# Kernel optimization log

Hardware: AMD Instinct MI355X
Metric: run time of the kernel (lower is better)

The kernel has to match this reference:

```python
import jax, jax.numpy as jnp
import numpy as np

D_MODEL = 1024
NHEAD = 16
D_K = D_MODEL // NHEAD


def setup_inputs() -> dict:
    key = jax.random.key(0)
    ks = jax.random.split(key, 10)
    B, S = 2, 2048
    x = jax.random.normal(ks[0], (B, S, D_MODEL), dtype=jnp.float32)
    # sorted 1-D coordinate grid in [0,1], shape [S,1,1] so coords.shape[1]==1
    coords = jnp.sort(jax.random.uniform(ks[1], (S, 1, 1), dtype=jnp.float32), axis=0)
    sc = 1.0 / np.sqrt(D_MODEL)
    Wq = jax.random.normal(ks[2], (D_MODEL, D_MODEL), dtype=jnp.float32) * sc
    bq = jnp.zeros((D_MODEL,), jnp.float32)
    Wk = jax.random.normal(ks[3], (D_MODEL, D_MODEL), dtype=jnp.float32) * sc
    bk = jnp.zeros((D_MODEL,), jnp.float32)
    Wv = jax.random.normal(ks[4], (D_MODEL, D_MODEL), dtype=jnp.float32) * sc
    bv = jnp.zeros((D_MODEL,), jnp.float32)
    Wo = jax.random.normal(ks[5], (D_MODEL, D_MODEL), dtype=jnp.float32) * sc
    bo = jnp.zeros((D_MODEL,), jnp.float32)
    return {"x": x, "coords": coords, "Wq": Wq, "bq": bq, "Wk": Wk, "bk": bk,
            "Wv": Wv, "bv": bv, "Wo": Wo, "bo": bo}


def _split_heads(t):  # [B,S,D] -> [B,H,S,Dk]
    B, S, _ = t.shape
    return t.reshape(B, S, NHEAD, D_K).transpose(0, 2, 1, 3)


def reference(x, coords, Wq, bq, Wk, bk, Wv, bv, Wo, bo):
    B, S, _ = x.shape
    Q = _split_heads(x @ Wq.T + bq)
    K = _split_heads(x @ Wk.T + bk)
    V = _split_heads(x @ Wv.T + bv)

    scale = jnp.sqrt(jnp.float32(D_K))
    scores = jnp.einsum('bhld,bhsd->bhls', Q, K) / scale  # [B,H,S,S]

    # trapezoidal quadrature weights from coord grid: [S-1] -> broadcast shapes
    dc = jnp.abs(coords[1:] - coords[:-1]).reshape(1, 1, 1, S - 1)  # key-axis

    # custom trapezoidal softmax
    e = jnp.exp(scores - jnp.max(scores, axis=-1, keepdims=True))
    denom = jnp.sum(0.5 * dc * (e[..., 1:] + e[..., :-1]), axis=-1, keepdims=True)
    aw = e / denom  # [B,H,S,S]

    dcv = dc.reshape(1, 1, S - 1, 1)  # value-axis weighting
    o1 = jnp.einsum('bhls,bhsd->bhld', aw[..., 1:], dcv * V[:, :, 1:, :])
    o2 = jnp.einsum('bhls,bhsd->bhld', aw[..., :-1], dcv * V[:, :, :-1, :])
    out = 0.5 * (o1 + o2)  # [B,H,S,Dk]

    out = out.transpose(0, 2, 1, 3).reshape(B, S, D_MODEL)
    return out @ Wo.T + bo
```

## Files before the change

kernel.cpp:

```cpp
#include <hip/hip_runtime.h>

#define DM 1024
#define NHEAD 16
#define DK 64
#define QLD 3072

typedef short bf16x8 __attribute__((ext_vector_type(8)));
typedef float f32x4 __attribute__((ext_vector_type(4)));

__device__ __forceinline__ unsigned short f2bf(float f) {
  union { float f; unsigned u; } v; v.f = f;
  return (unsigned short)((v.u + 0x7fffu + ((v.u >> 16) & 1u)) >> 16);
}
__device__ __forceinline__ float bf2f(unsigned short h) {
  union { unsigned u; float f; } v; v.u = ((unsigned)h) << 16; return v.f;
}
__device__ __forceinline__ float fexp2(float x) {
  float r; asm("v_exp_f32 %0, %1" : "=v"(r) : "v"(x)); return r;
}

__device__ __forceinline__ void gld16(const void* g, void* l) {
  __builtin_amdgcn_global_load_lds((const __attribute__((address_space(1))) void*)g,
                                   (__attribute__((address_space(3))) void*)l, 16, 0, 0);
}

__device__ __forceinline__ int kappa(int p) {
  return (p & 32) + (((p & 7) >> 2) << 4) + (((p >> 3) & 3) << 2) + (p & 3);
}

__global__ void k_prep(const float* __restrict__ x, const float* __restrict__ Wq,
                       const float* __restrict__ Wk, const float* __restrict__ Wv,
                       const float* __restrict__ Wo, const float* __restrict__ bq,
                       const float* __restrict__ bk, const float* __restrict__ bv,
                       const float* __restrict__ coords,
                       unsigned short* __restrict__ xb, unsigned short* __restrict__ Wcat,
                       unsigned short* __restrict__ Wob, float* __restrict__ bcat,
                       float* __restrict__ tw, unsigned short* __restrict__ twb,
                       int M, int S, float QS) {
  const int nx = M * DM / 4;
  const int nw = DM * DM / 4;
  const int total = nx + 4 * nw;
  int gid = blockIdx.x * 256 + threadIdx.x;

  auto conv4 = [&](const float* src, unsigned short* dst, int idx, float sc) {
    float4 v = *(const float4*)(src + idx * 4);
    ushort4 o;
    o.x = f2bf(v.x * sc); o.y = f2bf(v.y * sc);
    o.z = f2bf(v.z * sc); o.w = f2bf(v.w * sc);
    *(ushort4*)(dst + idx * 4) = o;
  };

  if (gid < nx) { conv4(x, xb, gid, 1.0f); return; }
  if (gid < nx + nw) { conv4(Wq, Wcat, gid - nx, QS); return; }
  if (gid < nx + 2 * nw) { conv4(Wk, Wcat + DM * DM, gid - nx - nw, 1.0f); return; }
  if (gid < nx + 3 * nw) { conv4(Wv, Wcat + 2 * DM * DM, gid - nx - 2 * nw, 1.0f); return; }
  if (gid < total) { conv4(Wo, Wob, gid - nx - 3 * nw, 1.0f); return; }

  int r = gid - total;
  if (r < 3 * DM) {
    float v = (r < DM) ? bq[r] * QS : (r < 2 * DM ? bk[r - DM] : bv[r - 2 * DM]);
    bcat[r] = v;
    return;
  }
  r -= 3 * DM;
  if (r < S) {
    auto twval = [&](int k) {
      float a = (k > 0)     ? fabsf(coords[k] - coords[k - 1]) : 0.f;
      float b = (k < S - 1) ? fabsf(coords[k + 1] - coords[k]) : 0.f;
      return 0.5f * (a + b);
    };
    tw[r] = twval(r);
    int key = (r & ~63) + kappa(r & 63);
    twb[r] = f2bf(twval(key));
  }
}

#define BM 128
#define BN 128
#define BKK 64

template<int OUTF32>
__global__ __launch_bounds__(256)
void gemm_bt(const unsigned short* __restrict__ A, const unsigned short* __restrict__ B,
             const float* __restrict__ bias, void* __restrict__ C,
             int M, int N, int K, int ldc) {
  __shared__ __align__(16) unsigned short sA[2][BM * BKK];
  __shared__ __align__(16) unsigned short sB[2][BN * BKK];
  const int tid = threadIdx.x;
  const int lane = tid & 63;
  const int wid = tid >> 6;
  const int rr = lane & 15, g = lane >> 4;
  const int nbn = N / BN;
  const int cpx = gridDim.x >> 3;
  const int bid = ((gridDim.x & 7) == 0) ? (blockIdx.x & 7) * cpx + (blockIdx.x >> 3)
                                         : blockIdx.x;
  const int bm = bid / nbn, bn = bid % nbn;
  const int wr = wid >> 1, wc = wid & 1;
  const int nkt = K / BKK;

  const unsigned short* Abase = A + (size_t)bm * BM * K;
  const unsigned short* Bbase = B + (size_t)bn * BN * K;

  auto stage = [&](int buf, int kt) {
#pragma unroll
    for (int j = 0; j < 4; ++j) {
      int o = j * 256 + tid;
      int row = o >> 3;
      int cb = ((o & 7) * 16) ^ ((row & 7) << 4);
      gld16((const char*)(Abase + (size_t)row * K + kt * BKK) + cb, &sA[buf][o * 8]);
      gld16((const char*)(Bbase + (size_t)row * K + kt * BKK) + cb, &sB[buf][o * 8]);
    }
  };

  f32x4 acc[4][4] = {};
  stage(0, 0);
  int cur = 0;
  const int sw = (rr & 7) << 4;
  for (int kt = 0; kt < nkt; ++kt) {
    __syncthreads();
    if (kt + 1 < nkt) stage(cur ^ 1, kt + 1);
    const char* a0 = (const char*)&sA[cur][(wr * 64) * BKK];
    const char* b0 = (const char*)&sB[cur][(wc * 64) * BKK];
#pragma unroll
    for (int kk = 0; kk < 2; ++kk) {
      const int co = (kk * 64 + g * 16);
      bf16x8 af[4], bfr[4];
#pragma unroll
      for (int m = 0; m < 4; ++m)
        af[m] = *(const bf16x8*)(a0 + (m * 16 + rr) * 128 + (co ^ sw));
#pragma unroll
      for (int n = 0; n < 4; ++n)
        bfr[n] = *(const bf16x8*)(b0 + (n * 16 + rr) * 128 + (co ^ sw));
      __builtin_amdgcn_s_setprio(1);
#pragma unroll
      for (int m = 0; m < 4; ++m)
#pragma unroll
        for (int n = 0; n < 4; ++n)
          acc[m][n] = __builtin_amdgcn_mfma_f32_16x16x32_bf16(af[m], bfr[n], acc[m][n], 0, 0, 0);
      __builtin_amdgcn_s_setprio(0);
    }
    cur ^= 1;
  }

  const int crow0 = bm * BM + wr * 64;
  const int ccol0 = bn * BN + wc * 64;
#pragma unroll
  for (int n = 0; n < 4; ++n) {
    const int col = ccol0 + n * 16 + rr;
    const float bn_ = bias ? bias[col] : 0.f;
#pragma unroll
    for (int m = 0; m < 4; ++m)
#pragma unroll
      for (int r = 0; r < 4; ++r) {
        const int row = crow0 + m * 16 + g * 4 + r;
        float v = acc[m][n][r] + bn_;
        if (OUTF32) ((float*)C)[(size_t)row * ldc + col] = v;
        else ((unsigned short*)C)[(size_t)row * ldc + col] = f2bf(v);
      }
  }
}

__global__ __launch_bounds__(256)
void k_transpose(const unsigned short* __restrict__ V, const float* __restrict__ tw,
                 unsigned short* __restrict__ Vt, int S, int ld) {
  __shared__ __align__(16) unsigned short t[64][72];
  __shared__ float tws[64];
  const int nst = S / 64;
  int st = blockIdx.x % nst;
  int bh = blockIdx.x / nst;
  int h = bh & (NHEAD - 1), b = bh / NHEAD;
  const unsigned short* src = V + ((size_t)b * S + st * 64) * ld + h * DK;
  unsigned short* dst = Vt + (size_t)bh * DK * S + st * 64;
  int tid = threadIdx.x;
  if (tid < 64) tws[tid] = tw[st * 64 + tid];
#pragma unroll
  for (int i = 0; i < 2; ++i) {
    int r = i * 32 + (tid >> 3);
    int c = (tid & 7) * 8;
    *(uint4*)&t[r][c] = *(const uint4*)&src[(size_t)r * ld + c];
  }
  __syncthreads();
#pragma unroll
  for (int i = 0; i < 2; ++i) {
    int d = i * 32 + (tid >> 3);
    int p0 = (tid & 7) * 8;
    unsigned short tmp[8];
#pragma unroll
    for (int j = 0; j < 8; ++j) {
      int kl = kappa(p0 + j);
      tmp[j] = f2bf(bf2f(t[kl][d]) * tws[kl]);
    }
    *(uint4*)&dst[(size_t)d * S + p0] = *(const uint4*)&tmp[0];
  }
}

__global__ __launch_bounds__(256)
void k_attn(const unsigned short* __restrict__ QKV, const unsigned short* __restrict__ Vt,
            const unsigned short* __restrict__ twb, unsigned short* __restrict__ O, int S) {
  __shared__ __align__(16) unsigned short sK[2][64 * 64];
  __shared__ __align__(16) unsigned short sV[2][64 * 64];
  const int tid = threadIdx.x, lane = tid & 63, wid = tid >> 6;
  const int rr = lane & 15, g = lane >> 4;
  const int nqt = S / 128;
  const int cpx = gridDim.x >> 3;
  const int swz = (blockIdx.x & 7) * cpx + (blockIdx.x >> 3);
  const int qt = swz % nqt;
  const int bh = swz / nqt;
  const int h = bh & (NHEAD - 1), b = bh / NHEAD;

  const unsigned short* Qbase = QKV + ((size_t)b * S + qt * 128 + wid * 32) * QLD + h * DK;
  const unsigned short* Kbase = QKV + (size_t)b * S * QLD + DM + h * DK;
  const unsigned short* Vbase = Vt + (size_t)bh * DK * S;

  bf16x8 aq[2][2];
#pragma unroll
  for (int qm = 0; qm < 2; ++qm) {
    aq[qm][0] = *(const bf16x8*)&Qbase[(size_t)(qm * 16 + rr) * QLD + g * 8];
    aq[qm][1] = *(const bf16x8*)&Qbase[(size_t)(qm * 16 + rr) * QLD + 32 + g * 8];
  }

  f32x4 acc[2][5] = {};
  const f32x4 z0 = {};

  auto stage = [&](int buf, int kt) {
#pragma unroll
    for (int j = 0; j < 2; ++j) {
      int o = j * 256 + tid;
      int row = o >> 3;
      int cb = ((o & 7) * 16) ^ ((row & 7) << 4);
      gld16((const char*)(Kbase + (size_t)(kt * 64 + row) * QLD) + cb, &sK[buf][o * 8]);
      gld16((const char*)(Vbase + (size_t)row * S + kt * 64) + cb, &sV[buf][o * 8]);
    }
  };

  stage(0, 0);
  int cur = 0;
  const int nkt = S / 64;
  for (int kt = 0; kt < nkt; ++kt) {
    __syncthreads();
    if (kt + 1 < nkt) stage(cur ^ 1, kt + 1);

    f32x4 s[2][4];
#pragma unroll
    for (int f = 0; f < 4; ++f) {
      const int row = f * 16 + rr;
      const int swzb = (row & 7) << 4;
      bf16x8 kA0 = *(const bf16x8*)((const char*)&sK[cur][row * 64] + ((g * 16) ^ swzb));
      bf16x8 kA1 = *(const bf16x8*)((const char*)&sK[cur][row * 64] + ((64 + g * 16) ^ swzb));
      __builtin_amdgcn_s_setprio(1);
#pragma unroll
      for (int qm = 0; qm < 2; ++qm) {
        f32x4 z = __builtin_amdgcn_mfma_f32_16x16x32_bf16(kA0, aq[qm][0], z0, 0, 0, 0);
        s[qm][f] = __builtin_amdgcn_mfma_f32_16x16x32_bf16(kA1, aq[qm][1], z, 0, 0, 0);
      }
      __builtin_amdgcn_s_setprio(0);
    }

#pragma unroll
    for (int qm = 0; qm < 2; ++qm)
#pragma unroll
      for (int f = 0; f < 4; ++f)
#pragma unroll
        for (int r = 0; r < 4; ++r)
          s[qm][f][r] = fexp2(s[qm][f][r]);

    bf16x8 pa[2][2];
#pragma unroll
    for (int qm = 0; qm < 2; ++qm)
#pragma unroll
      for (int kk = 0; kk < 2; ++kk) {
        union { bf16x8 v; unsigned u[4]; } pk;
        asm("v_cvt_pk_bf16_f32 %0, %1, %2" : "=v"(pk.u[0]) : "v"(s[qm][2*kk][0]),   "v"(s[qm][2*kk][1]));
        asm("v_cvt_pk_bf16_f32 %0, %1, %2" : "=v"(pk.u[1]) : "v"(s[qm][2*kk][2]),   "v"(s[qm][2*kk][3]));
        asm("v_cvt_pk_bf16_f32 %0, %1, %2" : "=v"(pk.u[2]) : "v"(s[qm][2*kk+1][0]), "v"(s[qm][2*kk+1][1]));
        asm("v_cvt_pk_bf16_f32 %0, %1, %2" : "=v"(pk.u[3]) : "v"(s[qm][2*kk+1][2]), "v"(s[qm][2*kk+1][3]));
        pa[qm][kk] = pk.v;
      }

    bf16x8 tw0 = *(const bf16x8*)&twb[kt * 64 + g * 8];
    bf16x8 tw1 = *(const bf16x8*)&twb[kt * 64 + 32 + g * 8];

#pragma unroll
    for (int kk = 0; kk < 2; ++kk) {
      __builtin_amdgcn_s_setprio(1);
#pragma unroll
      for (int n = 0; n < 4; ++n) {
        const int vrow = n * 16 + rr;
        const int cb = (kk * 64 + g * 16) ^ ((vrow & 7) << 4);
        bf16x8 bv = *(const bf16x8*)((const char*)&sV[cur][vrow * 64] + cb);
#pragma unroll
        for (int qm = 0; qm < 2; ++qm)
          acc[qm][n] = __builtin_amdgcn_mfma_f32_16x16x32_bf16(pa[qm][kk], bv, acc[qm][n], 0, 0, 0);
      }
#pragma unroll
      for (int qm = 0; qm < 2; ++qm)
        acc[qm][4] = __builtin_amdgcn_mfma_f32_16x16x32_bf16(pa[qm][kk], kk ? tw1 : tw0, acc[qm][4], 0, 0, 0);
      __builtin_amdgcn_s_setprio(0);
    }
    cur ^= 1;
  }

  unsigned short* Ob = O + ((size_t)b * S + qt * 128 + wid * 32) * DM + h * DK;
#pragma unroll
  for (int qm = 0; qm < 2; ++qm)
#pragma unroll
    for (int n = 0; n < 4; ++n)
#pragma unroll
      for (int r = 0; r < 4; ++r) {
        const int q = qm * 16 + g * 4 + r;
        const int d = n * 16 + rr;
        Ob[(size_t)q * DM + d] = f2bf(acc[qm][n][r] / acc[qm][4][r]);
      }
}

extern "C" void kernel_launch(void* const* d_in, const int* in_sizes, int n_in,
                              void* d_out, int out_size, void* d_ws, size_t ws_size,
                              hipStream_t stream) {
  const float* x      = (const float*)d_in[0];
  const float* coords = (const float*)d_in[1];
  const float* Wq = (const float*)d_in[2];
  const float* bq = (const float*)d_in[3];
  const float* Wk = (const float*)d_in[4];
  const float* bk = (const float*)d_in[5];
  const float* Wv = (const float*)d_in[6];
  const float* bv = (const float*)d_in[7];
  const float* Wo = (const float*)d_in[8];
  const float* bo = (const float*)d_in[9];

  const int S = in_sizes[1];
  const int B = in_sizes[0] / (S * DM);
  const int M = B * S;
  const float QS = 0.18033688011112042f;

  char* w = (char*)d_ws;
  size_t off = 0;
  unsigned short* xb   = (unsigned short*)(w + off); off += (size_t)M * DM * 2;
  unsigned short* Wcat = (unsigned short*)(w + off); off += (size_t)3 * DM * DM * 2;
  unsigned short* Wob  = (unsigned short*)(w + off); off += (size_t)DM * DM * 2;
  unsigned short* QKVb = (unsigned short*)(w + off); off += (size_t)M * QLD * 2;
  unsigned short* Vtb  = (unsigned short*)(w + off); off += (size_t)M * DM * 2;
  float* tw  = (float*)(w + off); off += (size_t)S * 4;
  unsigned short* twb = (unsigned short*)(w + off); off += (size_t)S * 2;
  float* bcat = (float*)(w + off); off += (size_t)3 * DM * 4;
  unsigned short* Ob = xb;
  (void)ws_size; (void)n_in; (void)out_size;

  {
    int nx = M * DM / 4, nw = DM * DM / 4;
    int total = nx + 4 * nw;
    int tail = 3 * DM + S;
    int gridp = total / 256 + (tail + 255) / 256;
    k_prep<<<gridp, 256, 0, stream>>>(x, Wq, Wk, Wv, Wo, bq, bk, bv, coords,
                                      xb, Wcat, Wob, bcat, tw, twb, M, S, QS);
  }

  gemm_bt<0><<<(M / BM) * (3 * DM / BN), 256, 0, stream>>>(xb, Wcat, bcat, QKVb, M, 3 * DM, DM, QLD);

  k_transpose<<<B * NHEAD * (S / 64), 256, 0, stream>>>(QKVb + 2 * DM, tw, Vtb, S, QLD);
  k_attn<<<B * NHEAD * (S / 128), 256, 0, stream>>>(QKVb, Vtb, twb, Ob, S);

  gemm_bt<1><<<(M / BM) * (DM / BN), 256, 0, stream>>>(Ob, Wob, bo, d_out, M, DM, DM, DM);
}
```

Baseline: 124.1 us.

## Split attention key tile across wave pairs with LDS reduction of partial outputs

Reorganizes the attention kernel so each wave handles 64 queries and half of each 64-key tile, instead of 32 queries over the full key tile. K and V fragments read from LDS are then reused across four query subtiles, which cuts LDS read traffic per MFMA. Partial numerators and denominators from the two key-halves are combined through shared memory at the end. This costs more accumulator registers and adds an extra reduction step with two barriers.

```diff
diff --git a/kernel.cpp b/kernel.cpp
--- a/kernel.cpp
+++ b/kernel.cpp
@@ -199,27 +199,30 @@
             const unsigned short* __restrict__ twb, unsigned short* __restrict__ O, int S) {
   __shared__ __align__(16) unsigned short sK[2][64 * 64];
   __shared__ __align__(16) unsigned short sV[2][64 * 64];
+  __shared__ float sden[2][64];
   const int tid = threadIdx.x, lane = tid & 63, wid = tid >> 6;
   const int rr = lane & 15, g = lane >> 4;
+  const int qg = wid >> 1, kg = wid & 1;
   const int nqt = S / 128;
   const int cpx = gridDim.x >> 3;
-  const int swz = (blockIdx.x & 7) * cpx + (blockIdx.x >> 3);
-  const int qt = swz % nqt;
-  const int bh = swz / nqt;
+  const int swzb_ = (blockIdx.x & 7) * cpx + (blockIdx.x >> 3);
+  const int qt = swzb_ % nqt;
+  const int bh = swzb_ / nqt;
   const int h = bh & (NHEAD - 1), b = bh / NHEAD;
 
-  const unsigned short* Qbase = QKV + ((size_t)b * S + qt * 128 + wid * 32) * QLD + h * DK;
+  const unsigned short* Qbase = QKV + ((size_t)b * S + qt * 128 + qg * 64) * QLD + h * DK;
   const unsigned short* Kbase = QKV + (size_t)b * S * QLD + DM + h * DK;
   const unsigned short* Vbase = Vt + (size_t)bh * DK * S;
 
-  bf16x8 aq[2][2];
-#pragma unroll
-  for (int qm = 0; qm < 2; ++qm) {
-    aq[qm][0] = *(const bf16x8*)&Qbase[(size_t)(qm * 16 + rr) * QLD + g * 8];
-    aq[qm][1] = *(const bf16x8*)&Qbase[(size_t)(qm * 16 + rr) * QLD + 32 + g * 8];
-  }
-
-  f32x4 acc[2][5] = {};
+  bf16x8 aq[4][2];
+#pragma unroll
+  for (int qsub = 0; qsub < 4; ++qsub) {
+    aq[qsub][0] = *(const bf16x8*)&Qbase[(size_t)(qsub * 16 + rr) * QLD + g * 8];
+    aq[qsub][1] = *(const bf16x8*)&Qbase[(size_t)(qsub * 16 + rr) * QLD + 32 + g * 8];
+  }
+
+  f32x4 acc[4][4] = {};
+  f32x4 den[4] = {};
   const f32x4 z0 = {};
 
   auto stage = [&](int buf, int kt) {
@@ -240,77 +243,95 @@
     __syncthreads();
     if (kt + 1 < nkt) stage(cur ^ 1, kt + 1);
 
-    f32x4 s[2][4];
-#pragma unroll
-    for (int f = 0; f < 4; ++f) {
-      const int row = f * 16 + rr;
-      const int swzb = (row & 7) << 4;
-      bf16x8 kA0 = *(const bf16x8*)((const char*)&sK[cur][row * 64] + ((g * 16) ^ swzb));
-      bf16x8 kA1 = *(const bf16x8*)((const char*)&sK[cur][row * 64] + ((64 + g * 16) ^ swzb));
-      __builtin_amdgcn_s_setprio(1);
-#pragma unroll
-      for (int qm = 0; qm < 2; ++qm) {
-        f32x4 z = __builtin_amdgcn_mfma_f32_16x16x32_bf16(kA0, aq[qm][0], z0, 0, 0, 0);
-        s[qm][f] = __builtin_amdgcn_mfma_f32_16x16x32_bf16(kA1, aq[qm][1], z, 0, 0, 0);
+    bf16x8 kA[2][2];
+#pragma unroll
+    for (int fi = 0; fi < 2; ++fi) {
+      const int row = (kg * 2 + fi) * 16 + rr;
+      const int swr = (row & 7) << 4;
+      kA[fi][0] = *(const bf16x8*)((const char*)&sK[cur][row * 64] + ((g * 16) ^ swr));
+      kA[fi][1] = *(const bf16x8*)((const char*)&sK[cur][row * 64] + ((64 + g * 16) ^ swr));
+    }
+
+    f32x4 s[4][2];
+    __builtin_amdgcn_s_setprio(1);
+#pragma unroll
+    for (int qsub = 0; qsub < 4; ++qsub)
+#pragma unroll
+      for (int fi = 0; fi < 2; ++fi) {
+        f32x4 z = __builtin_amdgcn_mfma_f32_16x16x32_bf16(kA[fi][0], aq[qsub][0], z0, 0, 0, 0);
+        s[qsub][fi] = __builtin_amdgcn_mfma_f32_16x16x32_bf16(kA[fi][1], aq[qsub][1], z, 0, 0, 0);
       }
-      __builtin_amdgcn_s_setprio(0);
-    }
-
-#pragma unroll
-    for (int qm = 0; qm < 2; ++qm)
-#pragma unroll
-      for (int f = 0; f < 4; ++f)
+    __builtin_amdgcn_s_setprio(0);
+
+#pragma unroll
+    for (int qsub = 0; qsub < 4; ++qsub)
+#pragma unroll
+      for (int fi = 0; fi < 2; ++fi)
 #pragma unroll
         for (int r = 0; r < 4; ++r)
-          s[qm][f][r] = fexp2(s[qm][f][r]);
-
-    bf16x8 pa[2][2];
-#pragma unroll
-    for (int qm = 0; qm < 2; ++qm)
-#pragma unroll
-      for (int kk = 0; kk < 2; ++kk) {
-        union { bf16x8 v; unsigned u[4]; } pk;
-        asm("v_cvt_pk_bf16_f32 %0, %1, %2" : "=v"(pk.u[0]) : "v"(s[qm][2*kk][0]),   "v"(s[qm][2*kk][1]));
-        asm("v_cvt_pk_bf16_f32 %0, %1, %2" : "=v"(pk.u[1]) : "v"(s[qm][2*kk][2]),   "v"(s[qm][2*kk][3]));
-        asm("v_cvt_pk_bf16_f32 %0, %1, %2" : "=v"(pk.u[2]) : "v"(s[qm][2*kk+1][0]), "v"(s[qm][2*kk+1][1]));
-        asm("v_cvt_pk_bf16_f32 %0, %1, %2" : "=v"(pk.u[3]) : "v"(s[qm][2*kk+1][2]), "v"(s[qm][2*kk+1][3]));
-        pa[qm][kk] = pk.v;
+          s[qsub][fi][r] = fexp2(s[qsub][fi][r]);
+
+    bf16x8 pa[4];
+#pragma unroll
+    for (int qsub = 0; qsub < 4; ++qsub) {
+      union { bf16x8 v; unsigned u[4]; } pk;
+      asm("v_cvt_pk_bf16_f32 %0, %1, %2" : "=v"(pk.u[0]) : "v"(s[qsub][0][0]), "v"(s[qsub][0][1]));
+      asm("v_cvt_pk_bf16_f32 %0, %1, %2" : "=v"(pk.u[1]) : "v"(s[qsub][0][2]), "v"(s[qsub][0][3]));
+      asm("v_cvt_pk_bf16_f32 %0, %1, %2" : "=v"(pk.u[2]) : "v"(s[qsub][1][0]), "v"(s[qsub][1][1]));
+      asm("v_cvt_pk_bf16_f32 %0, %1, %2" : "=v"(pk.u[3]) : "v"(s[qsub][1][2]), "v"(s[qsub][1][3]));
+      pa[qsub] = pk.v;
+    }
+
+    bf16x8 twf = *(const bf16x8*)&twb[kt * 64 + kg * 32 + g * 8];
+
+    __builtin_amdgcn_s_setprio(1);
+#pragma unroll
+    for (int n = 0; n < 4; ++n) {
+      const int vrow = n * 16 + rr;
+      const int cb = (kg * 64 + g * 16) ^ ((vrow & 7) << 4);
+      bf16x8 bv = *(const bf16x8*)((const char*)&sV[cur][vrow * 64] + cb);
+#pragma unroll
+      for (int qsub = 0; qsub < 4; ++qsub)
+        acc[qsub][n] = __builtin_amdgcn_mfma_f32_16x16x32_bf16(pa[qsub], bv, acc[qsub][n], 0, 0, 0);
+    }
+#pragma unroll
+    for (int qsub = 0; qsub < 4; ++qsub)
+      den[qsub] = __builtin_amdgcn_mfma_f32_16x16x32_bf16(pa[qsub], twf, den[qsub], 0, 0, 0);
+    __builtin_amdgcn_s_setprio(0);
+    cur ^= 1;
+  }
+
+  float* red = (qg == 0) ? (float*)&sK[0][0] : (float*)&sV[0][0];
+  __syncthreads();
+#pragma unroll
+  for (int h2 = 0; h2 < 2; ++h2) {
+    const int qsub = 2 * (1 - kg) + h2;
+#pragma unroll
+    for (int n = 0; n < 4; ++n)
+#pragma unroll
+      for (int r = 0; r < 4; ++r)
+        red[(qsub * 16 + g * 4 + r) * 64 + n * 16 + rr] = acc[qsub][n][r];
+    if (rr == 0)
+#pragma unroll
+      for (int r = 0; r < 4; ++r)
+        sden[qg][qsub * 16 + g * 4 + r] = den[qsub][r];
+  }
+  __syncthreads();
+  unsigned short* Ob = O + ((size_t)b * S + qt * 128 + qg * 64) * DM + h * DK;
+#pragma unroll
+  for (int h2 = 0; h2 < 2; ++h2) {
+    const int qsub = 2 * kg + h2;
+#pragma unroll
+    for (int r = 0; r < 4; ++r) {
+      const int q = qsub * 16 + g * 4 + r;
+      const float dsum = den[qsub][r] + sden[qg][q];
+#pragma unroll
+      for (int n = 0; n < 4; ++n) {
+        const float num = acc[qsub][n][r] + red[q * 64 + n * 16 + rr];
+        Ob[(size_t)q * DM + n * 16 + rr] = f2bf(num / dsum);
       }
-
-    bf16x8 tw0 = *(const bf16x8*)&twb[kt * 64 + g * 8];
-    bf16x8 tw1 = *(const bf16x8*)&twb[kt * 64 + 32 + g * 8];
-
-#pragma unroll
-    for (int kk = 0; kk < 2; ++kk) {
-      __builtin_amdgcn_s_setprio(1);
-#pragma unroll
-      for (int n = 0; n < 4; ++n) {
-        const int vrow = n * 16 + rr;
-        const int cb = (kk * 64 + g * 16) ^ ((vrow & 7) << 4);
-        bf16x8 bv = *(const bf16x8*)((const char*)&sV[cur][vrow * 64] + cb);
-#pragma unroll
-        for (int qm = 0; qm < 2; ++qm)
-          acc[qm][n] = __builtin_amdgcn_mfma_f32_16x16x32_bf16(pa[qm][kk], bv, acc[qm][n], 0, 0, 0);
-      }
-#pragma unroll
-      for (int qm = 0; qm < 2; ++qm)
-        acc[qm][4] = __builtin_amdgcn_mfma_f32_16x16x32_bf16(pa[qm][kk], kk ? tw1 : tw0, acc[qm][4], 0, 0, 0);
-      __builtin_amdgcn_s_setprio(0);
-    }
-    cur ^= 1;
-  }
-
-  unsigned short* Ob = O + ((size_t)b * S + qt * 128 + wid * 32) * DM + h * DK;
-#pragma unroll
-  for (int qm = 0; qm < 2; ++qm)
-#pragma unroll
-    for (int n = 0; n < 4; ++n)
-#pragma unroll
-      for (int r = 0; r < 4; ++r) {
-        const int q = qm * 16 + g * 4 + r;
-        const int d = n * 16 + rr;
-        Ob[(size_t)q * DM + d] = f2bf(acc[qm][n][r] / acc[qm][4][r]);
-      }
+    }
+  }
 }
 
 extern "C" void kernel_launch(void* const* d_in, const int* in_sizes, int n_in,
```

After: 355.9 us. +186.9%, slower.
